# Kernel optimization log

Hardware: AMD Instinct MI355X
Metric: run time of the kernel (lower is better)

Reference implementation:

```python
import jax, jax.numpy as jnp
import numpy as np

N, F_IN, E, DIM, G, C = 50000, 128, 800000, 64, 128, 10
BN_EPS = 1e-5


def setup_inputs() -> dict:
    key = jax.random.key(0)
    ks = jax.random.split(key, 24)
    x = jax.random.normal(ks[0], (N, F_IN), dtype=jnp.float32)
    edge_index = jax.random.randint(ks[1], (2, E), 0, N, dtype=jnp.int32)
    batch = jnp.sort(jax.random.randint(ks[2], (N,), 0, G, dtype=jnp.int32))

    def lin(k, fan_in, shape):
        b = 1.0 / np.sqrt(fan_in)
        return jax.random.uniform(k, shape, jnp.float32, -b, b)

    # layer 1 MLP: [F_IN->DIM], [DIM->DIM]
    W1a, b1a = lin(ks[3], F_IN, (F_IN, DIM)), lin(ks[4], F_IN, (DIM,))
    W1b, b1b = lin(ks[5], DIM, (DIM, DIM)), lin(ks[6], DIM, (DIM,))
    # layers 2-5 MLPs stacked: [4, DIM, DIM]
    Wa = jnp.stack([lin(jax.random.fold_in(ks[7], i), DIM, (DIM, DIM)) for i in range(4)])
    ba = jnp.stack([lin(jax.random.fold_in(ks[8], i), DIM, (DIM,)) for i in range(4)])
    Wb = jnp.stack([lin(jax.random.fold_in(ks[9], i), DIM, (DIM, DIM)) for i in range(4)])
    bb = jnp.stack([lin(jax.random.fold_in(ks[10], i), DIM, (DIM,)) for i in range(4)])
    gammas = jnp.ones((5, DIM), jnp.float32)
    betas = jnp.zeros((5, DIM), jnp.float32)
    fc1_w, fc1_b = lin(ks[11], DIM, (DIM, DIM)), lin(ks[12], DIM, (DIM,))
    fc2_w, fc2_b = lin(ks[13], DIM, (DIM, C)), lin(ks[14], DIM, (C,))
    return dict(x=x, edge_index=edge_index, batch=batch,
                W1a=W1a, b1a=b1a, W1b=W1b, b1b=b1b,
                Wa=Wa, ba=ba, Wb=Wb, bb=bb,
                gammas=gammas, betas=betas,
                fc1_w=fc1_w, fc1_b=fc1_b, fc2_w=fc2_w, fc2_b=fc2_b)


def _gin_conv(x, edge_index, W1, b1, W2, b2):
    # PyG GINConv (eps=0): MLP((1+eps)*x + scatter_add of source feats at targets)
    agg = jax.ops.segment_sum(x[edge_index[0]], edge_index[1], num_segments=N)
    h = x + agg
    h = jnp.maximum(h @ W1 + b1, 0.0) @ W2 + b2
    return h


def _bn(h, gamma, beta):
    # BatchNorm1d, training mode (batch statistics, biased variance)
    mean = h.mean(axis=0)
    var = h.var(axis=0)
    return (h - mean) * jax.lax.rsqrt(var + BN_EPS) * gamma + beta


def reference(x, edge_index, batch, W1a, b1a, W1b, b1b, Wa, ba, Wb, bb,
              gammas, betas, fc1_w, fc1_b, fc2_w, fc2_b):
    h = jnp.maximum(_gin_conv(x, edge_index, W1a, b1a, W1b, b1b), 0.0)
    h = _bn(h, gammas[0], betas[0])
    for i in range(4):
        h = jnp.maximum(_gin_conv(h, edge_index, Wa[i], ba[i], Wb[i], bb[i]), 0.0)
        h = _bn(h, gammas[i + 1], betas[i + 1])
    pooled = jax.ops.segment_sum(h, batch, num_segments=G)  # global_add_pool -> [G, DIM]
    z = jnp.maximum(pooled @ fc1_w + fc1_b, 0.0)
    z = z @ fc2_w + fc2_b
    return jax.nn.log_softmax(z, axis=-1)
```

## Files before the change

### kernel.cpp

```cpp
#include <hip/hip_runtime.h>
#include <hip/hip_fp16.h>


constexpr int N = 50000;
constexpr int E = 800000;
constexpr int G = 128;
constexpr int MAXDEG = 64;
constexpr float BN_EPS = 1e-5f;

__device__ inline float4 ld4(const float* p) { return *(const float4*)p; }
__device__ inline void st4(float* p, float4 v) { *(float4*)p = v; }

__device__ inline void acc8(float* a, float4 raw) {
    const __half2* h2 = (const __half2*)&raw;
#pragma unroll
    for (int i = 0; i < 4; i++) {
        float2 f2 = __half22float2(h2[i]);
        a[2 * i] += f2.x; a[2 * i + 1] += f2.y;
    }
}

union HF2 { __half2 h2[2]; float2 f2; };

__global__ __launch_bounds__(256) void count_fill_kernel(
    const int* __restrict__ ei, int* __restrict__ deg, int* __restrict__ ell)
{
    int e = blockIdx.x * 256 + threadIdx.x;
    if (e < E) {
        int s = ei[e];
        int d = ei[E + e];
        int slot = atomicAdd(&deg[d], 1);
        if (slot < MAXDEG) ell[d * MAXDEG + slot] = s;
    }
}

__global__ __launch_bounds__(256) void pad_kernel(
    const int* __restrict__ deg, int* __restrict__ ell)
{
    int n = blockIdx.x * 256 + threadIdx.x;
    if (n < N) {
        int dgc = min(deg[n], MAXDEG);
        int p = (dgc + 3) & ~3;
        for (int s = dgc; s < p; s++) ell[n * MAXDEG + s] = N;
    }
}

__global__ __launch_bounds__(256) void xw_kernel(
    const float* __restrict__ x, const float* __restrict__ W, __half* __restrict__ out)
{
    int tid = threadIdx.x;
    int ty = tid >> 4, tx = tid & 15;
    int base = blockIdx.x * 64;

    float acc[4][4];
#pragma unroll
    for (int r = 0; r < 4; r++)
#pragma unroll
        for (int cc = 0; cc < 4; cc++) acc[r][cc] = 0.f;

    int rr[4];
#pragma unroll
    for (int r = 0; r < 4; r++) rr[r] = min(base + 4 * ty + r, N - 1);

#pragma unroll 4
    for (int c = 0; c < 128; c++) {
        float4 w4 = ld4(W + c * 64 + 4 * tx);
#pragma unroll
        for (int r = 0; r < 4; r++) {
            float a = x[(size_t)rr[r] * 128 + c];
            acc[r][0] += a * w4.x; acc[r][1] += a * w4.y;
            acc[r][2] += a * w4.z; acc[r][3] += a * w4.w;
        }
    }
#pragma unroll
    for (int r = 0; r < 4; r++) {
        int node = base + 4 * ty + r;
        if (node < N) {
            HF2 u;
            u.h2[0] = __floats2half2_rn(acc[r][0], acc[r][1]);
            u.h2[1] = __floats2half2_rn(acc[r][2], acc[r][3]);
            *(float2*)(out + (size_t)node * 64 + 4 * tx) = u.f2;
        }
    }
}

__global__ __launch_bounds__(64) void reduce_stats_kernel(
    const float* __restrict__ partials, float* __restrict__ stats, int nb)
{
    int c = blockIdx.x;
    int lane = threadIdx.x;
    float s = 0.f;
    for (int i = lane; i < nb; i += 64)
        s += partials[(size_t)i * 128 + c];
#pragma unroll
    for (int off = 32; off > 0; off >>= 1)
        s += __shfl_down(s, off, 64);
    if (lane == 0) stats[c] = s;
}

template <bool FIRST>
__global__ __launch_bounds__(256) void layer_kernel(
    const __half* __restrict__ hin, const int* __restrict__ ell, const int* __restrict__ deg,
    const float* __restrict__ statsPrev, const float* __restrict__ gamma, const float* __restrict__ beta,
    const float* __restrict__ bias0,
    const float* __restrict__ W1, const float* __restrict__ b1,
    const float* __restrict__ W2, const float* __restrict__ b2,
    __half* __restrict__ hout, float* __restrict__ statsPart)
{
    __shared__ float sV[64 * 68];
    __shared__ float sStat[128];

    int tid = threadIdx.x, lane = tid & 63, wv = tid >> 6;
    if (tid < 128) sStat[tid] = 0.f;

    int base = blockIdx.x * 64;
    int n8 = lane >> 3, f = lane & 7;

    float sc[8], sh[8], b0[8];
    if constexpr (FIRST) {
#pragma unroll
        for (int q = 0; q < 2; q++) {
            float4 b4 = ld4(bias0 + 8 * f + 4 * q);
            b0[4 * q + 0] = b4.x; b0[4 * q + 1] = b4.y;
            b0[4 * q + 2] = b4.z; b0[4 * q + 3] = b4.w;
        }
    } else {
#pragma unroll
        for (int q = 0; q < 2; q++) {
            float4 s1 = ld4(statsPrev + 8 * f + 4 * q);
            float4 s2 = ld4(statsPrev + 64 + 8 * f + 4 * q);
            float4 g4 = ld4(gamma + 8 * f + 4 * q);
            float4 be4 = ld4(beta + 8 * f + 4 * q);
            float m[4] = { s1.x / N, s1.y / N, s1.z / N, s1.w / N };
            float v2[4] = { s2.x / N, s2.y / N, s2.z / N, s2.w / N };
            float gg[4] = { g4.x, g4.y, g4.z, g4.w };
            float bb4[4] = { be4.x, be4.y, be4.z, be4.w };
#pragma unroll
            for (int i = 0; i < 4; i++) {
                float s = gg[i] * rsqrtf(v2[i] - m[i] * m[i] + BN_EPS);
                sc[4 * q + i] = s;
                sh[4 * q + i] = bb4[i] - m[i] * s;
            }
        }
    }

#pragma unroll
    for (int kk = 0; kk < 2; kk++) {
        int node = base + wv * 16 + kk * 8 + n8;
        int nd = (node < N) ? node : N;
        int dg = (node < N) ? deg[node] : 0;
        int dgc = min(dg, MAXDEG);
        int p = (dgc + 3) & ~3;
        const int* row = ell + (size_t)nd * MAXDEG;

        float a0[8], a1[8], a2[8], a3[8];
#pragma unroll
        for (int i = 0; i < 8; i++) { a0[i] = 0.f; a1[i] = 0.f; a2[i] = 0.f; a3[i] = 0.f; }

        float4 rown = ld4((const float*)(hin + (size_t)nd * 64 + 8 * f));
        for (int j = 0; j < p; j += 4) {
            int4 iv = *(const int4*)(row + j);
            float4 r0 = ld4((const float*)(hin + (size_t)iv.x * 64 + 8 * f));
            float4 r1 = ld4((const float*)(hin + (size_t)iv.y * 64 + 8 * f));
            float4 r2 = ld4((const float*)(hin + (size_t)iv.z * 64 + 8 * f));
            float4 r3 = ld4((const float*)(hin + (size_t)iv.w * 64 + 8 * f));
            acc8(a0, r0); acc8(a1, r1); acc8(a2, r2); acc8(a3, r3);
        }
        acc8(a0, rown);

        float v[8];
#pragma unroll
        for (int i = 0; i < 8; i++) {
            float s = (a0[i] + a1[i]) + (a2[i] + a3[i]);
            if constexpr (FIRST) {
                v[i] = fmaxf(s + b0[i], 0.f);
            } else {
                v[i] = sc[i] * s + (float)(1 + dg) * sh[i];
            }
        }
        int ridx = wv * 16 + kk * 8 + n8;
        st4(sV + ridx * 68 + 8 * f,     make_float4(v[0], v[1], v[2], v[3]));
        st4(sV + ridx * 68 + 8 * f + 4, make_float4(v[4], v[5], v[6], v[7]));
    }
    __syncthreads();

    int ty = tid >> 4, tx = tid & 15;

    if constexpr (!FIRST) {
        float acc[4][4];
#pragma unroll
        for (int cc = 0; cc < 4; cc++) {
            float b = b1[4 * tx + cc];
            acc[0][cc] = b; acc[1][cc] = b; acc[2][cc] = b; acc[3][cc] = b;
        }
#pragma unroll 4
        for (int c = 0; c < 64; c++) {
            float4 w4 = ld4(W1 + c * 64 + 4 * tx);
#pragma unroll
            for (int r = 0; r < 4; r++) {
                float a = sV[(4 * ty + r) * 68 + c];
                acc[r][0] += a * w4.x; acc[r][1] += a * w4.y;
                acc[r][2] += a * w4.z; acc[r][3] += a * w4.w;
            }
        }
        __syncthreads();
#pragma unroll
        for (int r = 0; r < 4; r++)
            st4(sV + (4 * ty + r) * 68 + 4 * tx,
                make_float4(fmaxf(acc[r][0], 0.f), fmaxf(acc[r][1], 0.f),
                            fmaxf(acc[r][2], 0.f), fmaxf(acc[r][3], 0.f)));
        __syncthreads();
    }

    float acc[4][4];
#pragma unroll
    for (int cc = 0; cc < 4; cc++) {
        float b = b2[4 * tx + cc];
        acc[0][cc] = b; acc[1][cc] = b; acc[2][cc] = b; acc[3][cc] = b;
    }
#pragma unroll 4
    for (int c = 0; c < 64; c++) {
        float4 w4 = ld4(W2 + c * 64 + 4 * tx);
#pragma unroll
        for (int r = 0; r < 4; r++) {
            float a = sV[(4 * ty + r) * 68 + c];
            acc[r][0] += a * w4.x; acc[r][1] += a * w4.y;
            acc[r][2] += a * w4.z; acc[r][3] += a * w4.w;
        }
    }
#pragma unroll
    for (int r = 0; r < 4; r++) {
        int node = base + 4 * ty + r;
        if (node < N) {
            acc[r][0] = fmaxf(acc[r][0], 0.f); acc[r][1] = fmaxf(acc[r][1], 0.f);
            acc[r][2] = fmaxf(acc[r][2], 0.f); acc[r][3] = fmaxf(acc[r][3], 0.f);
            HF2 u;
            u.h2[0] = __floats2half2_rn(acc[r][0], acc[r][1]);
            u.h2[1] = __floats2half2_rn(acc[r][2], acc[r][3]);
            *(float2*)(hout + (size_t)node * 64 + 4 * tx) = u.f2;
        } else {
            acc[r][0] = acc[r][1] = acc[r][2] = acc[r][3] = 0.f;
        }
    }
#pragma unroll
    for (int cc = 0; cc < 4; cc++) {
        float s = 0.f, q = 0.f;
#pragma unroll
        for (int r = 0; r < 4; r++) { s += acc[r][cc]; q += acc[r][cc] * acc[r][cc]; }
        atomicAdd(&sStat[4 * tx + cc], s);
        atomicAdd(&sStat[64 + 4 * tx + cc], q);
    }
    __syncthreads();
    if (tid < 128) statsPart[(size_t)blockIdx.x * 128 + tid] = sStat[tid];
}

__global__ __launch_bounds__(256) void pool_head_kernel(
    const __half* __restrict__ h, const int* __restrict__ batch,
    const float* __restrict__ stats, const float* __restrict__ gamma, const float* __restrict__ beta,
    const float* __restrict__ fc1w, const float* __restrict__ fc1b,
    const float* __restrict__ fc2w, const float* __restrict__ fc2b,
    float* __restrict__ out)
{
    __shared__ float sacc[4][64];
    __shared__ float sp[64];
    __shared__ float sz[64];
    __shared__ float so[10];

    int g = blockIdx.x;
    int lane = threadIdx.x & 63, wv = threadIdx.x >> 6;

    int start, end;
    {
        int lo = 0, hi = N;
        while (lo < hi) { int mid = (lo + hi) >> 1; if (batch[mid] < g) lo = mid + 1; else hi = mid; }
        start = lo;
        lo = start; hi = N;
        while (lo < hi) { int mid = (lo + hi) >> 1; if (batch[mid] < g + 1) lo = mid + 1; else hi = mid; }
        end = lo;
    }

    float acc = 0.f;
    for (int node = start + wv; node < end; node += 4)
        acc += __half2float(h[(size_t)node * 64 + lane]);
    sacc[wv][lane] = acc;
    __syncthreads();

    if (wv == 0) {
        float mean = stats[lane] * (1.f / N);
        float var  = stats[64 + lane] * (1.f / N) - mean * mean;
        float sc = gamma[lane] * rsqrtf(var + BN_EPS);
        float sh = beta[lane] - mean * sc;
        float t = sacc[0][lane] + sacc[1][lane] + sacc[2][lane] + sacc[3][lane];
        sp[lane] = sc * t + (float)(end - start) * sh;
    }
    __syncthreads();
    if (wv == 0) {
        float a = fc1b[lane];
#pragma unroll
        for (int c = 0; c < 64; c++) a += sp[c] * fc1w[c * 64 + lane];
        sz[lane] = fmaxf(a, 0.f);
    }
    __syncthreads();
    if (wv == 0 && lane < 10) {
        float z = fc2b[lane];
#pragma unroll
        for (int j = 0; j < 64; j++) z += sz[j] * fc2w[j * 10 + lane];
        so[lane] = z;
    }
    __syncthreads();
    if (wv == 0 && lane < 10) {
        float m = -1e30f;
#pragma unroll
        for (int c = 0; c < 10; c++) m = fmaxf(m, so[c]);
        float s = 0.f;
#pragma unroll
        for (int c = 0; c < 10; c++) s += expf(so[c] - m);
        out[g * 10 + lane] = so[lane] - m - logf(s);
    }
}

extern "C" void kernel_launch(void* const* d_in, const int* in_sizes, int n_in,
                              void* d_out, int out_size, void* d_ws, size_t ws_size,
                              hipStream_t stream)
{
    const float* x    = (const float*)d_in[0];
    const int*   ei   = (const int*)  d_in[1];
    const int*   batch= (const int*)  d_in[2];
    const float* W1a  = (const float*)d_in[3];
    const float* b1a  = (const float*)d_in[4];
    const float* W1b  = (const float*)d_in[5];
    const float* b1b  = (const float*)d_in[6];
    const float* Wa   = (const float*)d_in[7];
    const float* ba   = (const float*)d_in[8];
    const float* Wb   = (const float*)d_in[9];
    const float* bb   = (const float*)d_in[10];
    const float* gammas = (const float*)d_in[11];
    const float* betas  = (const float*)d_in[12];
    const float* fc1w = (const float*)d_in[13];
    const float* fc1b = (const float*)d_in[14];
    const float* fc2w = (const float*)d_in[15];
    const float* fc2b = (const float*)d_in[16];
    float* out = (float*)d_out;

    char* w = (char*)d_ws;
    int*    deg     = (int*)w;
    float*  stats   = (float*)(w + 200000);
    int*    ell     = (int*)(w + 202752);
    __half* bufA    = (__half*)(w + 13002752);
    __half* bufB    = (__half*)(w + 19403008);
    float*  partials= (float*)(w + 25803136);

    hipMemsetAsync(d_ws, 0, 200000, stream);
    hipMemsetAsync(bufA + (size_t)N * 64, 0, 128, stream);
    hipMemsetAsync(bufB + (size_t)N * 64, 0, 128, stream);

    count_fill_kernel<<<(E + 255) / 256, 256, 0, stream>>>(ei, deg, ell);
    pad_kernel<<<(N + 255) / 256, 256, 0, stream>>>(deg, ell);
    xw_kernel<<<(N + 63) / 64, 256, 0, stream>>>(x, W1a, bufA);

    int nb = (N + 63) / 64;

    layer_kernel<true><<<nb, 256, 0, stream>>>(
        bufA, ell, deg, nullptr, nullptr, nullptr, b1a,
        nullptr, nullptr, W1b, b1b, bufB, partials);
    reduce_stats_kernel<<<128, 64, 0, stream>>>(partials, stats, nb);

    layer_kernel<false><<<nb, 256, 0, stream>>>(
        bufB, ell, deg, stats, gammas, betas, nullptr,
        Wa, ba, Wb, bb, bufA, partials);
    reduce_stats_kernel<<<128, 64, 0, stream>>>(partials, stats + 128, nb);

    layer_kernel<false><<<nb, 256, 0, stream>>>(
        bufA, ell, deg, stats + 128, gammas + 64, betas + 64, nullptr,
        Wa + 4096, ba + 64, Wb + 4096, bb + 64, bufB, partials);
    reduce_stats_kernel<<<128, 64, 0, stream>>>(partials, stats + 256, nb);

    layer_kernel<false><<<nb, 256, 0, stream>>>(
        bufB, ell, deg, stats + 256, gammas + 128, betas + 128, nullptr,
        Wa + 8192, ba + 128, Wb + 8192, bb + 128, bufA, partials);
    reduce_stats_kernel<<<128, 64, 0, stream>>>(partials, stats + 384, nb);

    layer_kernel<false><<<nb, 256, 0, stream>>>(
        bufA, ell, deg, stats + 384, gammas + 192, betas + 192, nullptr,
        Wa + 12288, ba + 192, Wb + 12288, bb + 192, bufB, partials);
    reduce_stats_kernel<<<128, 64, 0, stream>>>(partials, stats + 512, nb);

    pool_head_kernel<<<G, 256, 0, stream>>>(
        bufB, batch, stats + 512, gammas + 256, betas + 256,
        fc1w, fc1b, fc2w, fc2b, out);
}
```

Measured before the change: 450.2 us.

## Sort nodes by degree, compress ELL indices to 16-bit, unroll gathers by 8

Builds a degree histogram, scans it, and creates a permutation so each block processes nodes of similar degree, which cuts wavefront divergence in the gather loop. ELL neighbor indices are stored as unsigned short, halving index traffic and ELL size, and the gather loop issues 8 row loads per iteration with padding rounded up to 8. The price is three extra setup kernels, one of them a serial single-thread scan, plus an extra perm lookup per node. The 16-bit indices only hold because N=50000 fits under 65536.

Result: slower. 659.4 us (+46.5%).

```diff
diff --git a/kernel.cpp b/kernel.cpp
--- a/kernel.cpp
+++ b/kernel.cpp
@@ -23,25 +23,48 @@
 union HF2 { __half2 h2[2]; float2 f2; };
 
 __global__ __launch_bounds__(256) void count_fill_kernel(
-    const int* __restrict__ ei, int* __restrict__ deg, int* __restrict__ ell)
+    const int* __restrict__ ei, int* __restrict__ deg, unsigned short* __restrict__ ell)
 {
     int e = blockIdx.x * 256 + threadIdx.x;
     if (e < E) {
         int s = ei[e];
         int d = ei[E + e];
         int slot = atomicAdd(&deg[d], 1);
-        if (slot < MAXDEG) ell[d * MAXDEG + slot] = s;
+        if (slot < MAXDEG) ell[d * MAXDEG + slot] = (unsigned short)s;
     }
 }
 
 __global__ __launch_bounds__(256) void pad_kernel(
-    const int* __restrict__ deg, int* __restrict__ ell)
+    const int* __restrict__ deg, unsigned short* __restrict__ ell)
 {
     int n = blockIdx.x * 256 + threadIdx.x;
     if (n < N) {
         int dgc = min(deg[n], MAXDEG);
-        int p = (dgc + 3) & ~3;
-        for (int s = dgc; s < p; s++) ell[n * MAXDEG + s] = N;
+        int p = (dgc + 7) & ~7;
+        for (int s = dgc; s < p; s++) ell[n * MAXDEG + s] = (unsigned short)N;
+    }
+}
+
+__global__ __launch_bounds__(256) void hist_kernel(
+    const int* __restrict__ deg, int* __restrict__ hist)
+{
+    int n = blockIdx.x * 256 + threadIdx.x;
+    if (n < N) atomicAdd(&hist[min(deg[n], MAXDEG)], 1);
+}
+
+__global__ void scan_kernel(int* __restrict__ hist)
+{
+    int run = 0;
+    for (int b = 0; b <= MAXDEG; b++) { int h = hist[b]; hist[b] = run; run += h; }
+}
+
+__global__ __launch_bounds__(256) void scatter_perm_kernel(
+    const int* __restrict__ deg, int* __restrict__ hist, int* __restrict__ perm)
+{
+    int n = blockIdx.x * 256 + threadIdx.x;
+    if (n < N) {
+        int slot = atomicAdd(&hist[min(deg[n], MAXDEG)], 1);
+        perm[slot] = n;
     }
 }
 
@@ -100,7 +123,8 @@
 
 template <bool FIRST>
 __global__ __launch_bounds__(256) void layer_kernel(
-    const __half* __restrict__ hin, const int* __restrict__ ell, const int* __restrict__ deg,
+    const __half* __restrict__ hin, const unsigned short* __restrict__ ell,
+    const int* __restrict__ deg, const int* __restrict__ perm,
     const float* __restrict__ statsPrev, const float* __restrict__ gamma, const float* __restrict__ beta,
     const float* __restrict__ bias0,
     const float* __restrict__ W1, const float* __restrict__ b1,
@@ -146,25 +170,34 @@
 
 #pragma unroll
     for (int kk = 0; kk < 2; kk++) {
-        int node = base + wv * 16 + kk * 8 + n8;
-        int nd = (node < N) ? node : N;
-        int dg = (node < N) ? deg[node] : 0;
+        int slot = base + wv * 16 + kk * 8 + n8;
+        int nd = (slot < N) ? perm[slot] : N;
+        int dg = (slot < N) ? deg[nd] : 0;
         int dgc = min(dg, MAXDEG);
-        int p = (dgc + 3) & ~3;
-        const int* row = ell + (size_t)nd * MAXDEG;
+        int p = (dgc + 7) & ~7;
+        const unsigned short* row = ell + (size_t)nd * MAXDEG;
 
         float a0[8], a1[8], a2[8], a3[8];
 #pragma unroll
         for (int i = 0; i < 8; i++) { a0[i] = 0.f; a1[i] = 0.f; a2[i] = 0.f; a3[i] = 0.f; }
 
         float4 rown = ld4((const float*)(hin + (size_t)nd * 64 + 8 * f));
-        for (int j = 0; j < p; j += 4) {
-            int4 iv = *(const int4*)(row + j);
-            float4 r0 = ld4((const float*)(hin + (size_t)iv.x * 64 + 8 * f));
-            float4 r1 = ld4((const float*)(hin + (size_t)iv.y * 64 + 8 * f));
-            float4 r2 = ld4((const float*)(hin + (size_t)iv.z * 64 + 8 * f));
-            float4 r3 = ld4((const float*)(hin + (size_t)iv.w * 64 + 8 * f));
+        for (int j = 0; j < p; j += 8) {
+            uint4 iv = *(const uint4*)(row + j);
+            int i0 = iv.x & 0xFFFF, i1 = (int)(iv.x >> 16);
+            int i2 = iv.y & 0xFFFF, i3 = (int)(iv.y >> 16);
+            int i4 = iv.z & 0xFFFF, i5 = (int)(iv.z >> 16);
+            int i6 = iv.w & 0xFFFF, i7 = (int)(iv.w >> 16);
+            float4 r0 = ld4((const float*)(hin + (size_t)i0 * 64 + 8 * f));
+            float4 r1 = ld4((const float*)(hin + (size_t)i1 * 64 + 8 * f));
+            float4 r2 = ld4((const float*)(hin + (size_t)i2 * 64 + 8 * f));
+            float4 r3 = ld4((const float*)(hin + (size_t)i3 * 64 + 8 * f));
+            float4 r4 = ld4((const float*)(hin + (size_t)i4 * 64 + 8 * f));
+            float4 r5 = ld4((const float*)(hin + (size_t)i5 * 64 + 8 * f));
+            float4 r6 = ld4((const float*)(hin + (size_t)i6 * 64 + 8 * f));
+            float4 r7 = ld4((const float*)(hin + (size_t)i7 * 64 + 8 * f));
             acc8(a0, r0); acc8(a1, r1); acc8(a2, r2); acc8(a3, r3);
+            acc8(a0, r4); acc8(a1, r5); acc8(a2, r6); acc8(a3, r7);
         }
         acc8(a0, rown);
 
@@ -230,8 +263,9 @@
     }
 #pragma unroll
     for (int r = 0; r < 4; r++) {
-        int node = base + 4 * ty + r;
-        if (node < N) {
+        int slot = base + 4 * ty + r;
+        if (slot < N) {
+            int node = perm[slot];
             acc[r][0] = fmaxf(acc[r][0], 0.f); acc[r][1] = fmaxf(acc[r][1], 0.f);
             acc[r][2] = fmaxf(acc[r][2], 0.f); acc[r][3] = fmaxf(acc[r][3], 0.f);
             HF2 u;
@@ -343,45 +377,50 @@
     float* out = (float*)d_out;
 
     char* w = (char*)d_ws;
-    int*    deg     = (int*)w;
-    float*  stats   = (float*)(w + 200000);
-    int*    ell     = (int*)(w + 202752);
-    __half* bufA    = (__half*)(w + 13002752);
-    __half* bufB    = (__half*)(w + 19403008);
-    float*  partials= (float*)(w + 25803136);
-
-    hipMemsetAsync(d_ws, 0, 200000, stream);
+    int*            deg      = (int*)w;
+    int*            hist     = (int*)(w + 200000);
+    float*          stats    = (float*)(w + 200704);
+    unsigned short* ell      = (unsigned short*)(w + 203264);
+    int*            perm     = (int*)(w + 6603264);
+    __half*         bufA     = (__half*)(w + 6803328);
+    __half*         bufB     = (__half*)(w + 13203456);
+    float*          partials = (float*)(w + 19603584);
+
+    hipMemsetAsync(d_ws, 0, 200260, stream);
     hipMemsetAsync(bufA + (size_t)N * 64, 0, 128, stream);
     hipMemsetAsync(bufB + (size_t)N * 64, 0, 128, stream);
 
     count_fill_kernel<<<(E + 255) / 256, 256, 0, stream>>>(ei, deg, ell);
     pad_kernel<<<(N + 255) / 256, 256, 0, stream>>>(deg, ell);
+    hist_kernel<<<(N + 255) / 256, 256, 0, stream>>>(deg, hist);
+    scan_kernel<<<1, 1, 0, stream>>>(hist);
+    scatter_perm_kernel<<<(N + 255) / 256, 256, 0, stream>>>(deg, hist, perm);
     xw_kernel<<<(N + 63) / 64, 256, 0, stream>>>(x, W1a, bufA);
 
     int nb = (N + 63) / 64;
 
     layer_kernel<true><<<nb, 256, 0, stream>>>(
-        bufA, ell, deg, nullptr, nullptr, nullptr, b1a,
+        bufA, ell, deg, perm, nullptr, nullptr, nullptr, b1a,
         nullptr, nullptr, W1b, b1b, bufB, partials);
     reduce_stats_kernel<<<128, 64, 0, stream>>>(partials, stats, nb);
 
     layer_kernel<false><<<nb, 256, 0, stream>>>(
-        bufB, ell, deg, stats, gammas, betas, nullptr,
+        bufB, ell, deg, perm, stats, gammas, betas, nullptr,
         Wa, ba, Wb, bb, bufA, partials);
     reduce_stats_kernel<<<128, 64, 0, stream>>>(partials, stats + 128, nb);
 
     layer_kernel<false><<<nb, 256, 0, stream>>>(
-        bufA, ell, deg, stats + 128, gammas + 64, betas + 64, nullptr,
+        bufA, ell, deg, perm, stats + 128, gammas + 64, betas + 64, nullptr,
         Wa + 4096, ba + 64, Wb + 4096, bb + 64, bufB, partials);
     reduce_stats_kernel<<<128, 64, 0, stream>>>(partials, stats + 256, nb);
 
     layer_kernel<false><<<nb, 256, 0, stream>>>(
-        bufB, ell, deg, stats + 256, gammas + 128, betas + 128, nullptr,
+        bufB, ell, deg, perm, stats + 256, gammas + 128, betas + 128, nullptr,
         Wa + 8192, ba + 128, Wb + 8192, bb + 128, bufA, partials);
     reduce_stats_kernel<<<128, 64, 0, stream>>>(partials, stats + 384, nb);
 
     layer_kernel<false><<<nb, 256, 0, stream>>>(
-        bufA, ell, deg, stats + 384, gammas + 192, betas + 192, nullptr,
+        bufA, ell, deg, perm, stats + 384, gammas + 192, betas + 192, nullptr,
         Wa + 12288, ba + 192, Wb + 12288, bb + 192, bufB, partials);
     reduce_stats_kernel<<<128, 64, 0, stream>>>(partials, stats + 512, nb);
 
```

## Use 16-bit ELL indices and half2 accumulation with 8-wide gather unroll

Applied to the files above, without the earlier changes.

Node indices in the ELL adjacency are stored as unsigned short, which fits because N is under 65536; this halves index traffic. The neighbor gather is unrolled to 8 rows per iteration, with the next index vector prefetched, and sums are accumulated with packed half2 adds across 8 partial accumulators instead of converting every value to fp32. Padding changes to multiples of 8. Accumulating in fp16 cuts ALU work but can lose precision over up to 64 neighbors.

After: 439.6 us. -2.4%, faster.

```diff
diff --git a/kernel.cpp b/kernel.cpp
--- a/kernel.cpp
+++ b/kernel.cpp
@@ -11,37 +11,28 @@
 __device__ inline float4 ld4(const float* p) { return *(const float4*)p; }
 __device__ inline void st4(float* p, float4 v) { *(float4*)p = v; }
 
-__device__ inline void acc8(float* a, float4 raw) {
-    const __half2* h2 = (const __half2*)&raw;
-#pragma unroll
-    for (int i = 0; i < 4; i++) {
-        float2 f2 = __half22float2(h2[i]);
-        a[2 * i] += f2.x; a[2 * i + 1] += f2.y;
-    }
-}
-
 union HF2 { __half2 h2[2]; float2 f2; };
 
 __global__ __launch_bounds__(256) void count_fill_kernel(
-    const int* __restrict__ ei, int* __restrict__ deg, int* __restrict__ ell)
+    const int* __restrict__ ei, int* __restrict__ deg, unsigned short* __restrict__ ell)
 {
     int e = blockIdx.x * 256 + threadIdx.x;
     if (e < E) {
         int s = ei[e];
         int d = ei[E + e];
         int slot = atomicAdd(&deg[d], 1);
-        if (slot < MAXDEG) ell[d * MAXDEG + slot] = s;
+        if (slot < MAXDEG) ell[d * MAXDEG + slot] = (unsigned short)s;
     }
 }
 
 __global__ __launch_bounds__(256) void pad_kernel(
-    const int* __restrict__ deg, int* __restrict__ ell)
+    const int* __restrict__ deg, unsigned short* __restrict__ ell)
 {
     int n = blockIdx.x * 256 + threadIdx.x;
     if (n < N) {
         int dgc = min(deg[n], MAXDEG);
-        int p = (dgc + 3) & ~3;
-        for (int s = dgc; s < p; s++) ell[n * MAXDEG + s] = N;
+        int p = (dgc + 7) & ~7;
+        for (int s = dgc; s < p; s++) ell[n * MAXDEG + s] = (unsigned short)N;
     }
 }
 
@@ -100,7 +91,8 @@
 
 template <bool FIRST>
 __global__ __launch_bounds__(256) void layer_kernel(
-    const __half* __restrict__ hin, const int* __restrict__ ell, const int* __restrict__ deg,
+    const __half* __restrict__ hin, const unsigned short* __restrict__ ell,
+    const int* __restrict__ deg,
     const float* __restrict__ statsPrev, const float* __restrict__ gamma, const float* __restrict__ beta,
     const float* __restrict__ bias0,
     const float* __restrict__ W1, const float* __restrict__ b1,
@@ -150,32 +142,70 @@
         int nd = (node < N) ? node : N;
         int dg = (node < N) ? deg[node] : 0;
         int dgc = min(dg, MAXDEG);
-        int p = (dgc + 3) & ~3;
-        const int* row = ell + (size_t)nd * MAXDEG;
-
-        float a0[8], a1[8], a2[8], a3[8];
-#pragma unroll
-        for (int i = 0; i < 8; i++) { a0[i] = 0.f; a1[i] = 0.f; a2[i] = 0.f; a3[i] = 0.f; }
+        int p = (dgc + 7) & ~7;
+        const unsigned short* row = ell + (size_t)nd * MAXDEG;
+
+        __half2 ap[8][4];
+#pragma unroll
+        for (int r = 0; r < 8; r++)
+#pragma unroll
+            for (int k = 0; k < 4; k++) ap[r][k] = __half2(__float2half(0.f), __float2half(0.f));
 
         float4 rown = ld4((const float*)(hin + (size_t)nd * 64 + 8 * f));
-        for (int j = 0; j < p; j += 4) {
-            int4 iv = *(const int4*)(row + j);
-            float4 r0 = ld4((const float*)(hin + (size_t)iv.x * 64 + 8 * f));
-            float4 r1 = ld4((const float*)(hin + (size_t)iv.y * 64 + 8 * f));
-            float4 r2 = ld4((const float*)(hin + (size_t)iv.z * 64 + 8 * f));
-            float4 r3 = ld4((const float*)(hin + (size_t)iv.w * 64 + 8 * f));
-            acc8(a0, r0); acc8(a1, r1); acc8(a2, r2); acc8(a3, r3);
-        }
-        acc8(a0, rown);
-
+
+        if (p > 0) {
+            uint4 iv = *(const uint4*)(row);
+            for (int j = 0; j < p; j += 8) {
+                uint4 ivn = iv;
+                if (j + 8 < p) ivn = *(const uint4*)(row + j + 8);
+                int i0 = iv.x & 0xFFFF, i1 = (int)(iv.x >> 16);
+                int i2 = iv.y & 0xFFFF, i3 = (int)(iv.y >> 16);
+                int i4 = iv.z & 0xFFFF, i5 = (int)(iv.z >> 16);
+                int i6 = iv.w & 0xFFFF, i7 = (int)(iv.w >> 16);
+                float4 r0 = ld4((const float*)(hin + (size_t)i0 * 64 + 8 * f));
+                float4 r1 = ld4((const float*)(hin + (size_t)i1 * 64 + 8 * f));
+                float4 r2 = ld4((const float*)(hin + (size_t)i2 * 64 + 8 * f));
+                float4 r3 = ld4((const float*)(hin + (size_t)i3 * 64 + 8 * f));
+                float4 r4 = ld4((const float*)(hin + (size_t)i4 * 64 + 8 * f));
+                float4 r5 = ld4((const float*)(hin + (size_t)i5 * 64 + 8 * f));
+                float4 r6 = ld4((const float*)(hin + (size_t)i6 * 64 + 8 * f));
+                float4 r7 = ld4((const float*)(hin + (size_t)i7 * 64 + 8 * f));
+                iv = ivn;
+                const __half2* h0 = (const __half2*)&r0; const __half2* h1 = (const __half2*)&r1;
+                const __half2* h2 = (const __half2*)&r2; const __half2* h3 = (const __half2*)&r3;
+                const __half2* h4 = (const __half2*)&r4; const __half2* h5 = (const __half2*)&r5;
+                const __half2* h6 = (const __half2*)&r6; const __half2* h7 = (const __half2*)&r7;
+#pragma unroll
+                for (int k = 0; k < 4; k++) {
+                    ap[0][k] = __hadd2(ap[0][k], h0[k]);
+                    ap[1][k] = __hadd2(ap[1][k], h1[k]);
+                    ap[2][k] = __hadd2(ap[2][k], h2[k]);
+                    ap[3][k] = __hadd2(ap[3][k], h3[k]);
+                    ap[4][k] = __hadd2(ap[4][k], h4[k]);
+                    ap[5][k] = __hadd2(ap[5][k], h5[k]);
+                    ap[6][k] = __hadd2(ap[6][k], h6[k]);
+                    ap[7][k] = __hadd2(ap[7][k], h7[k]);
+                }
+            }
+        }
+
+        const __half2* ho = (const __half2*)&rown;
         float v[8];
 #pragma unroll
-        for (int i = 0; i < 8; i++) {
-            float s = (a0[i] + a1[i]) + (a2[i] + a3[i]);
+        for (int k = 0; k < 4; k++) {
+            float2 s = __half22float2(ho[k]);
+#pragma unroll
+            for (int r = 0; r < 8; r++) {
+                float2 fr = __half22float2(ap[r][k]);
+                s.x += fr.x; s.y += fr.y;
+            }
             if constexpr (FIRST) {
-                v[i] = fmaxf(s + b0[i], 0.f);
+                v[2 * k]     = fmaxf(s.x + b0[2 * k], 0.f);
+                v[2 * k + 1] = fmaxf(s.y + b0[2 * k + 1], 0.f);
             } else {
-                v[i] = sc[i] * s + (float)(1 + dg) * sh[i];
+                float dsh = (float)(1 + dg);
+                v[2 * k]     = sc[2 * k] * s.x + dsh * sh[2 * k];
+                v[2 * k + 1] = sc[2 * k + 1] * s.y + dsh * sh[2 * k + 1];
             }
         }
         int ridx = wv * 16 + kk * 8 + n8;
@@ -343,12 +373,12 @@
     float* out = (float*)d_out;
 
     char* w = (char*)d_ws;
-    int*    deg     = (int*)w;
-    float*  stats   = (float*)(w + 200000);
-    int*    ell     = (int*)(w + 202752);
-    __half* bufA    = (__half*)(w + 13002752);
-    __half* bufB    = (__half*)(w + 19403008);
-    float*  partials= (float*)(w + 25803136);
+    int*            deg      = (int*)w;
+    float*          stats    = (float*)(w + 200704);
+    unsigned short* ell      = (unsigned short*)(w + 203264);
+    __half*         bufA     = (__half*)(w + 6603264);
+    __half*         bufB     = (__half*)(w + 13003392);
+    float*          partials = (float*)(w + 19403520);
 
     hipMemsetAsync(d_ws, 0, 200000, stream);
     hipMemsetAsync(bufA + (size_t)N * 64, 0, 128, stream);
```

## Use 16-bit ELL indices, partitioned fill, and fp16 packed gather accumulation

Applied to the files above, without the earlier changes.

The neighbour list is stored as unsigned short indices (N fits in 16 bits) and pre-filled with 0xFFFF, which is clamped to the zero row, so the separate padding kernel is removed. The fill kernel is split into 8 destination partitions to localise atomics and scattered writes. Each thread now gathers two nodes at once with 8-wide index loads and accumulates in packed half2 adds. This cuts index traffic and instruction count, but half-precision accumulation over up to 64 neighbours loses accuracy, and each block reads the edge array 8 times.

Measured after the change: 440.6 us. -2.1%, faster.

```diff
diff --git a/kernel.cpp b/kernel.cpp
--- a/kernel.cpp
+++ b/kernel.cpp
@@ -6,42 +6,27 @@
 constexpr int E = 800000;
 constexpr int G = 128;
 constexpr int MAXDEG = 64;
+constexpr int NPART = 8;
+constexpr int PART_SZ = (N + NPART - 1) / NPART;
 constexpr float BN_EPS = 1e-5f;
 
 __device__ inline float4 ld4(const float* p) { return *(const float4*)p; }
 __device__ inline void st4(float* p, float4 v) { *(float4*)p = v; }
 
-__device__ inline void acc8(float* a, float4 raw) {
-    const __half2* h2 = (const __half2*)&raw;
-#pragma unroll
-    for (int i = 0; i < 4; i++) {
-        float2 f2 = __half22float2(h2[i]);
-        a[2 * i] += f2.x; a[2 * i + 1] += f2.y;
-    }
-}
-
 union HF2 { __half2 h2[2]; float2 f2; };
 
 __global__ __launch_bounds__(256) void count_fill_kernel(
-    const int* __restrict__ ei, int* __restrict__ deg, int* __restrict__ ell)
-{
-    int e = blockIdx.x * 256 + threadIdx.x;
+    const int* __restrict__ ei, int* __restrict__ deg, unsigned short* __restrict__ ell)
+{
+    int part = blockIdx.x & (NPART - 1);
+    int e = (blockIdx.x >> 3) * 256 + threadIdx.x;
     if (e < E) {
-        int s = ei[e];
         int d = ei[E + e];
-        int slot = atomicAdd(&deg[d], 1);
-        if (slot < MAXDEG) ell[d * MAXDEG + slot] = s;
-    }
-}
-
-__global__ __launch_bounds__(256) void pad_kernel(
-    const int* __restrict__ deg, int* __restrict__ ell)
-{
-    int n = blockIdx.x * 256 + threadIdx.x;
-    if (n < N) {
-        int dgc = min(deg[n], MAXDEG);
-        int p = (dgc + 3) & ~3;
-        for (int s = dgc; s < p; s++) ell[n * MAXDEG + s] = N;
+        if (d / PART_SZ == part) {
+            int s = ei[e];
+            int slot = atomicAdd(&deg[d], 1);
+            if (slot < MAXDEG) ell[(size_t)d * MAXDEG + slot] = (unsigned short)s;
+        }
     }
 }
 
@@ -100,7 +85,8 @@
 
 template <bool FIRST>
 __global__ __launch_bounds__(256) void layer_kernel(
-    const __half* __restrict__ hin, const int* __restrict__ ell, const int* __restrict__ deg,
+    const __half* __restrict__ hin, const unsigned short* __restrict__ ell,
+    const int* __restrict__ deg,
     const float* __restrict__ statsPrev, const float* __restrict__ gamma, const float* __restrict__ beta,
     const float* __restrict__ bias0,
     const float* __restrict__ W1, const float* __restrict__ b1,
@@ -144,43 +130,111 @@
         }
     }
 
-#pragma unroll
-    for (int kk = 0; kk < 2; kk++) {
-        int node = base + wv * 16 + kk * 8 + n8;
-        int nd = (node < N) ? node : N;
-        int dg = (node < N) ? deg[node] : 0;
-        int dgc = min(dg, MAXDEG);
-        int p = (dgc + 3) & ~3;
-        const int* row = ell + (size_t)nd * MAXDEG;
-
-        float a0[8], a1[8], a2[8], a3[8];
-#pragma unroll
-        for (int i = 0; i < 8; i++) { a0[i] = 0.f; a1[i] = 0.f; a2[i] = 0.f; a3[i] = 0.f; }
-
-        float4 rown = ld4((const float*)(hin + (size_t)nd * 64 + 8 * f));
-        for (int j = 0; j < p; j += 4) {
-            int4 iv = *(const int4*)(row + j);
-            float4 r0 = ld4((const float*)(hin + (size_t)iv.x * 64 + 8 * f));
-            float4 r1 = ld4((const float*)(hin + (size_t)iv.y * 64 + 8 * f));
-            float4 r2 = ld4((const float*)(hin + (size_t)iv.z * 64 + 8 * f));
-            float4 r3 = ld4((const float*)(hin + (size_t)iv.w * 64 + 8 * f));
-            acc8(a0, r0); acc8(a1, r1); acc8(a2, r2); acc8(a3, r3);
-        }
-        acc8(a0, rown);
-
-        float v[8];
-#pragma unroll
-        for (int i = 0; i < 8; i++) {
-            float s = (a0[i] + a1[i]) + (a2[i] + a3[i]);
+    {
+        int nodeA = base + wv * 16 + n8;
+        int nodeB = nodeA + 8;
+        int ndA = (nodeA < N) ? nodeA : N;
+        int ndB = (nodeB < N) ? nodeB : N;
+        int dgA = (nodeA < N) ? deg[nodeA] : 0;
+        int dgB = (nodeB < N) ? deg[nodeB] : 0;
+        int pA = (min(dgA, MAXDEG) + 7) & ~7;
+        int pB = (min(dgB, MAXDEG) + 7) & ~7;
+        int pm = max(pA, pB);
+        const unsigned short* rowA = ell + (size_t)ndA * MAXDEG;
+        const unsigned short* rowB = ell + (size_t)ndB * MAXDEG;
+
+        __half2 apA[4][4], apB[4][4];
+        __half2 z2 = __half2(__float2half(0.f), __float2half(0.f));
+#pragma unroll
+        for (int r = 0; r < 4; r++)
+#pragma unroll
+            for (int k = 0; k < 4; k++) { apA[r][k] = z2; apB[r][k] = z2; }
+
+        float4 rownA = ld4((const float*)(hin + (size_t)ndA * 64 + 8 * f));
+        float4 rownB = ld4((const float*)(hin + (size_t)ndB * 64 + 8 * f));
+
+        for (int j = 0; j < pm; j += 8) {
+            uint4 ivA = *(const uint4*)(rowA + j);
+            uint4 ivB = *(const uint4*)(rowB + j);
+            int a0 = min((int)(ivA.x & 0xFFFFu), N), a1 = min((int)(ivA.x >> 16), N);
+            int a2 = min((int)(ivA.y & 0xFFFFu), N), a3 = min((int)(ivA.y >> 16), N);
+            int a4 = min((int)(ivA.z & 0xFFFFu), N), a5 = min((int)(ivA.z >> 16), N);
+            int a6 = min((int)(ivA.w & 0xFFFFu), N), a7 = min((int)(ivA.w >> 16), N);
+            int b0i = min((int)(ivB.x & 0xFFFFu), N), b1i = min((int)(ivB.x >> 16), N);
+            int b2i = min((int)(ivB.y & 0xFFFFu), N), b3i = min((int)(ivB.y >> 16), N);
+            int b4i = min((int)(ivB.z & 0xFFFFu), N), b5i = min((int)(ivB.z >> 16), N);
+            int b6i = min((int)(ivB.w & 0xFFFFu), N), b7i = min((int)(ivB.w >> 16), N);
+            float4 rA0 = ld4((const float*)(hin + (size_t)a0 * 64 + 8 * f));
+            float4 rA1 = ld4((const float*)(hin + (size_t)a1 * 64 + 8 * f));
+            float4 rA2 = ld4((const float*)(hin + (size_t)a2 * 64 + 8 * f));
+            float4 rA3 = ld4((const float*)(hin + (size_t)a3 * 64 + 8 * f));
+            float4 rA4 = ld4((const float*)(hin + (size_t)a4 * 64 + 8 * f));
+            float4 rA5 = ld4((const float*)(hin + (size_t)a5 * 64 + 8 * f));
+            float4 rA6 = ld4((const float*)(hin + (size_t)a6 * 64 + 8 * f));
+            float4 rA7 = ld4((const float*)(hin + (size_t)a7 * 64 + 8 * f));
+            float4 rB0 = ld4((const float*)(hin + (size_t)b0i * 64 + 8 * f));
+            float4 rB1 = ld4((const float*)(hin + (size_t)b1i * 64 + 8 * f));
+            float4 rB2 = ld4((const float*)(hin + (size_t)b2i * 64 + 8 * f));
+            float4 rB3 = ld4((const float*)(hin + (size_t)b3i * 64 + 8 * f));
+            float4 rB4 = ld4((const float*)(hin + (size_t)b4i * 64 + 8 * f));
+            float4 rB5 = ld4((const float*)(hin + (size_t)b5i * 64 + 8 * f));
+            float4 rB6 = ld4((const float*)(hin + (size_t)b6i * 64 + 8 * f));
+            float4 rB7 = ld4((const float*)(hin + (size_t)b7i * 64 + 8 * f));
+            const __half2* hA0 = (const __half2*)&rA0; const __half2* hA1 = (const __half2*)&rA1;
+            const __half2* hA2 = (const __half2*)&rA2; const __half2* hA3 = (const __half2*)&rA3;
+            const __half2* hA4 = (const __half2*)&rA4; const __half2* hA5 = (const __half2*)&rA5;
+            const __half2* hA6 = (const __half2*)&rA6; const __half2* hA7 = (const __half2*)&rA7;
+            const __half2* hB0 = (const __half2*)&rB0; const __half2* hB1 = (const __half2*)&rB1;
+            const __half2* hB2 = (const __half2*)&rB2; const __half2* hB3 = (const __half2*)&rB3;
+            const __half2* hB4 = (const __half2*)&rB4; const __half2* hB5 = (const __half2*)&rB5;
+            const __half2* hB6 = (const __half2*)&rB6; const __half2* hB7 = (const __half2*)&rB7;
+#pragma unroll
+            for (int k = 0; k < 4; k++) {
+                apA[0][k] = __hadd2(apA[0][k], __hadd2(hA0[k], hA4[k]));
+                apA[1][k] = __hadd2(apA[1][k], __hadd2(hA1[k], hA5[k]));
+                apA[2][k] = __hadd2(apA[2][k], __hadd2(hA2[k], hA6[k]));
+                apA[3][k] = __hadd2(apA[3][k], __hadd2(hA3[k], hA7[k]));
+                apB[0][k] = __hadd2(apB[0][k], __hadd2(hB0[k], hB4[k]));
+                apB[1][k] = __hadd2(apB[1][k], __hadd2(hB1[k], hB5[k]));
+                apB[2][k] = __hadd2(apB[2][k], __hadd2(hB2[k], hB6[k]));
+                apB[3][k] = __hadd2(apB[3][k], __hadd2(hB3[k], hB7[k]));
+            }
+        }
+
+        const __half2* hoA = (const __half2*)&rownA;
+        const __half2* hoB = (const __half2*)&rownB;
+        float vA[8], vB[8];
+#pragma unroll
+        for (int k = 0; k < 4; k++) {
+            float2 sA = __half22float2(hoA[k]);
+            float2 sB = __half22float2(hoB[k]);
+#pragma unroll
+            for (int r = 0; r < 4; r++) {
+                float2 fa = __half22float2(apA[r][k]);
+                float2 fb = __half22float2(apB[r][k]);
+                sA.x += fa.x; sA.y += fa.y;
+                sB.x += fb.x; sB.y += fb.y;
+            }
             if constexpr (FIRST) {
-                v[i] = fmaxf(s + b0[i], 0.f);
+                vA[2 * k]     = fmaxf(sA.x + b0[2 * k], 0.f);
+                vA[2 * k + 1] = fmaxf(sA.y + b0[2 * k + 1], 0.f);
+                vB[2 * k]     = fmaxf(sB.x + b0[2 * k], 0.f);
+                vB[2 * k + 1] = fmaxf(sB.y + b0[2 * k + 1], 0.f);
             } else {
-                v[i] = sc[i] * s + (float)(1 + dg) * sh[i];
+                float dshA = (float)(1 + dgA);
+                float dshB = (float)(1 + dgB);
+                vA[2 * k]     = sc[2 * k] * sA.x + dshA * sh[2 * k];
+                vA[2 * k + 1] = sc[2 * k + 1] * sA.y + dshA * sh[2 * k + 1];
+                vB[2 * k]     = sc[2 * k] * sB.x + dshB * sh[2 * k];
+                vB[2 * k + 1] = sc[2 * k + 1] * sB.y + dshB * sh[2 * k + 1];
             }
         }
-        int ridx = wv * 16 + kk * 8 + n8;
-        st4(sV + ridx * 68 + 8 * f,     make_float4(v[0], v[1], v[2], v[3]));
-        st4(sV + ridx * 68 + 8 * f + 4, make_float4(v[4], v[5], v[6], v[7]));
+        int ridxA = wv * 16 + n8;
+        int ridxB = wv * 16 + 8 + n8;
+        st4(sV + ridxA * 68 + 8 * f,     make_float4(vA[0], vA[1], vA[2], vA[3]));
+        st4(sV + ridxA * 68 + 8 * f + 4, make_float4(vA[4], vA[5], vA[6], vA[7]));
+        st4(sV + ridxB * 68 + 8 * f,     make_float4(vB[0], vB[1], vB[2], vB[3]));
+        st4(sV + ridxB * 68 + 8 * f + 4, make_float4(vB[4], vB[5], vB[6], vB[7]));
     }
     __syncthreads();
 
@@ -343,19 +397,19 @@
     float* out = (float*)d_out;
 
     char* w = (char*)d_ws;
-    int*    deg     = (int*)w;
-    float*  stats   = (float*)(w + 200000);
-    int*    ell     = (int*)(w + 202752);
-    __half* bufA    = (__half*)(w + 13002752);
-    __half* bufB    = (__half*)(w + 19403008);
-    float*  partials= (float*)(w + 25803136);
-
-    hipMemsetAsync(d_ws, 0, 200000, stream);
+    int*            deg      = (int*)w;
+    float*          stats    = (float*)(w + 200704);
+    unsigned short* ell      = (unsigned short*)(w + 203264);
+    __half*         bufA     = (__half*)(w + 6603392);
+    __half*         bufB     = (__half*)(w + 13003520);
+    float*          partials = (float*)(w + 19403648);
+
+    hipMemsetAsync(deg, 0, 200000, stream);
+    hipMemsetAsync(ell, 0xFF, 6400128, stream);
     hipMemsetAsync(bufA + (size_t)N * 64, 0, 128, stream);
     hipMemsetAsync(bufB + (size_t)N * 64, 0, 128, stream);
 
-    count_fill_kernel<<<(E + 255) / 256, 256, 0, stream>>>(ei, deg, ell);
-    pad_kernel<<<(N + 255) / 256, 256, 0, stream>>>(deg, ell);
+    count_fill_kernel<<<NPART * ((E + 255) / 256), 256, 0, stream>>>(ei, deg, ell);
     xw_kernel<<<(N + 63) / 64, 256, 0, stream>>>(x, W1a, bufA);
 
     int nb = (N + 63) / 64;
```
